# Optimization experiments

Hardware: AMD Instinct MI355X
Metric: run time of the kernel (lower is better)

## Reference

```python
import jax, jax.numpy as jnp
import numpy as np
import math

B, N, M = 128, 32, 64           # batch, num_agents, num_other
OBS, ACT = 128, 16              # obs_input_dim, num_actions
D_QK = 128                      # obs_output_dim (== obs_output_dim_other)
D_AV = 64                       # obs_act_output_dim (== other)
F_IN = OBS + ACT                # obs_act_input_dim = 144


def _xavier(key, shape):
    fan_in, fan_out = shape[0], shape[1]
    limit = math.sqrt(6.0 / (fan_in + fan_out))
    return jax.random.uniform(key, shape, jnp.float32, -limit, limit)


def setup_inputs() -> dict:
    key = jax.random.key(0)
    ks = jax.random.split(key, 13)
    return {
        "states": jax.random.normal(ks[0], (B, N, OBS), jnp.float32),
        "policies": jax.random.uniform(ks[1], (B, N, ACT), jnp.float32),
        "actions": jax.random.uniform(ks[2], (B, N, ACT), jnp.float32),
        "states_other": jax.random.normal(ks[3], (B, M, OBS), jnp.float32),
        "actions_other": jax.random.uniform(ks[4], (B, M, ACT), jnp.float32),
        # weights stored as [in, out] (x @ W == nn.Linear without bias)
        "W_key": _xavier(ks[5], (OBS, D_QK)),
        "W_query": _xavier(ks[6], (OBS, D_QK)),
        "W_av": _xavier(ks[7], (F_IN, D_AV)),
        "W_key_other": _xavier(ks[8], (OBS, D_QK)),
        "W_query_other": _xavier(ks[9], (OBS, D_QK)),
        "W_av_other": _xavier(ks[10], (F_IN, D_AV)),
        "W_f1": _xavier(ks[11], (2 * D_AV, 64)),
        "W_f2": _xavier(ks[12], (64, 1)),
    }


def reference(states, policies, actions, states_other, actions_other,
              W_key, W_query, W_av, W_key_other, W_query_other,
              W_av_other, W_f1, W_f2):
    b, n, _ = states.shape
    obs_actions = jnp.concatenate([states, actions], axis=-1)   # [B,N,F_IN]
    obs_policy = jnp.concatenate([states, policies], axis=-1)   # [B,N,F_IN]

    key_obs = states @ W_key                                    # [B,N,D_QK]
    query_obs = states @ W_query                                # [B,N,D_QK]
    d_k = W_key.shape[1]
    weight = jax.nn.softmax(
        jnp.einsum('bid,bjd->bij', query_obs, key_obs) / math.sqrt(d_k), axis=-1)
    ret_weight = weight

    # place_policies is identity on (j,k): oap[b,j,k] = obs_policy[b,k] if j==k else obs_actions[b,k]
    eye = jnp.eye(n, dtype=states.dtype)[None, :, :, None]       # [1,N,N,1]
    oap = eye * obs_policy[:, None, :, :] + (1.0 - eye) * obs_actions[:, None, :, :]
    attention_values = jnp.tanh(oap @ W_av)                      # [B,N,N,D_AV] (j,k)

    # repeat-mul-sum == weighted reduction over k: wav[b,i,j,d] = sum_k w[b,i,k] av[b,j,k,d]
    wav = jnp.einsum('bik,bjkd->bijd', weight, attention_values)  # [B,N,N,D_AV]

    obs_actions_other = jnp.concatenate([states_other, actions_other], axis=-1)
    keys_other = states_other @ W_key_other                      # [B,M,D_QK]
    query_agent = states @ W_query_other                         # [B,N,D_QK]
    av_other = jnp.tanh(obs_actions_other @ W_av_other)          # [B,M,D_AV]
    d_k_o = W_key_other.shape[1]
    weight_other = jax.nn.softmax(
        jnp.einsum('bid,bmd->bim', query_agent, keys_other) / math.sqrt(d_k_o), axis=-1)
    wav_other = jnp.einsum('bim,bmd->bid', weight_other, av_other)  # [B,N,D_AV]

    # broadcast the per-agent other-branch features across the j axis for the concat
    wav_other_b = jnp.broadcast_to(wav_other[:, :, None, :], wav.shape[:-1] + (wav_other.shape[-1],))
    node_features = jnp.concatenate([wav, wav_other_b], axis=-1)  # [B,N,N,2*D_AV]

    h = jax.nn.leaky_relu(node_features @ W_f1, negative_slope=0.01)
    value = h @ W_f2                                              # [B,N,N,1]
    return value, ret_weight, weight_other
```

## Files before the change

kernel.cpp:

```cpp
#include <hip/hip_runtime.h>
#include <math.h>

#define WS_WQK   0
#define WS_WQKO  16384
#define WS_AVA   32768
#define WS_AVO   294912
#define WS_DPROJ 819200

#define INV_SQRT_DK 0.08838834764831845f

__device__ __forceinline__ float dot4(float4 a, float4 b) {
  return a.x*b.x + a.y*b.y + a.z*b.z + a.w*b.w;
}
__device__ __forceinline__ void fma4(float4& a, const float4 w, const float s) {
  a.x += w.x*s; a.y += w.y*s; a.z += w.z*s; a.w += w.w*s;
}

__global__ __launch_bounds__(256) void k1_pre(
    const float* __restrict__ g_states, const float* __restrict__ g_pol,
    const float* __restrict__ g_act, const float* __restrict__ g_so,
    const float* __restrict__ g_ao,
    const float* __restrict__ Wq, const float* __restrict__ Wk,
    const float* __restrict__ Wqo, const float* __restrict__ Wko,
    const float* __restrict__ W_av, const float* __restrict__ W_avo,
    const float* __restrict__ W_f1, float* __restrict__ ws)
{
  __shared__ __align__(16) float pool[8448];
  const int t = threadIdx.x;
  int blk = blockIdx.x;

  if (blk < 32) {
    const float* A; const float* Bm; float* O;
    if (blk < 16) { A = Wq;  Bm = Wk;  O = ws + WS_WQK; }
    else          { A = Wqo; Bm = Wko; O = ws + WS_WQKO; blk -= 16; }
    const int tr = (blk >> 2) << 5;
    const int tc = (blk & 3) << 5;
    float* sA = pool;
    float* sB = pool + 4224;
    const float4* a4 = (const float4*)(A + tr * 128);
    const float4* b4 = (const float4*)(Bm + tc * 128);
    #pragma unroll
    for (int u = 0; u < 4; ++u) {
      int f = t + u * 256;
      int r = f >> 5, c4 = f & 31;
      *(float4*)(sA + r*132 + c4*4) = a4[f];
      *(float4*)(sB + r*132 + c4*4) = b4[f];
    }
    __syncthreads();
    const int e = t & 31, cl0 = t >> 5;
    float acc[4] = {0,0,0,0};
    #pragma unroll 4
    for (int d4 = 0; d4 < 32; ++d4) {
      float4 bv = *(const float4*)(sB + e*132 + d4*4);
      #pragma unroll
      for (int rr = 0; rr < 4; ++rr) {
        float4 av = *(const float4*)(sA + (cl0 + rr*8)*132 + d4*4);
        acc[rr] += dot4(av, bv);
      }
    }
    #pragma unroll
    for (int rr = 0; rr < 4; ++rr)
      O[(tr + cl0 + rr*8)*128 + tc + e] = acc[rr];
    return;
  }
  blk -= 32;

  if (blk < 128) {
    const int b = blk;
    float* s_pre = pool;
    float* s_dl  = pool + 4224;
    {
      const int wv_  = t >> 6;
      const int ap   = wv_ & 1;
      const int rh   = wv_ >> 1;
      const int lane = t & 63;
      const float* gs = g_states + b*4096 + rh*16*128;
      const float* gt = (ap ? g_pol : g_act) + b*512 + rh*16*16;
      float acc[16];
      #pragma unroll
      for (int r = 0; r < 16; ++r) acc[r] = 0.f;
      #pragma unroll 4
      for (int c4 = 0; c4 < 32; ++c4) {
        const float w0 = W_av[(c4*4+0)*64 + lane];
        const float w1 = W_av[(c4*4+1)*64 + lane];
        const float w2 = W_av[(c4*4+2)*64 + lane];
        const float w3 = W_av[(c4*4+3)*64 + lane];
        #pragma unroll
        for (int r = 0; r < 16; ++r) {
          float4 sv = *(const float4*)(gs + r*128 + c4*4);
          acc[r] += sv.x*w0 + sv.y*w1 + sv.z*w2 + sv.w*w3;
        }
      }
      #pragma unroll
      for (int c4 = 0; c4 < 4; ++c4) {
        const float w0 = W_av[(128 + c4*4+0)*64 + lane];
        const float w1 = W_av[(128 + c4*4+1)*64 + lane];
        const float w2 = W_av[(128 + c4*4+2)*64 + lane];
        const float w3 = W_av[(128 + c4*4+3)*64 + lane];
        #pragma unroll
        for (int r = 0; r < 16; ++r) {
          float4 sv = *(const float4*)(gt + r*16 + c4*4);
          acc[r] += sv.x*w0 + sv.y*w1 + sv.z*w2 + sv.w*w3;
        }
      }
      #pragma unroll
      for (int r = 0; r < 16; ++r)
        s_pre[(rh*16 + r)*132 + ap*64 + lane] = acc[r];
    }
    __syncthreads();
    {
      const int r = t >> 3, d0 = (t & 7) << 3;
      float4 a0 = *(const float4*)(s_pre + r*132 + d0);
      float4 a1 = *(const float4*)(s_pre + r*132 + d0 + 4);
      float4 p0 = *(const float4*)(s_pre + r*132 + 64 + d0);
      float4 p1 = *(const float4*)(s_pre + r*132 + 64 + d0 + 4);
      float4 va0, va1, dl0, dl1;
      va0.x = tanhf(a0.x); va0.y = tanhf(a0.y); va0.z = tanhf(a0.z); va0.w = tanhf(a0.w);
      va1.x = tanhf(a1.x); va1.y = tanhf(a1.y); va1.z = tanhf(a1.z); va1.w = tanhf(a1.w);
      dl0.x = tanhf(p0.x) - va0.x; dl0.y = tanhf(p0.y) - va0.y;
      dl0.z = tanhf(p0.z) - va0.z; dl0.w = tanhf(p0.w) - va0.w;
      dl1.x = tanhf(p1.x) - va1.x; dl1.y = tanhf(p1.y) - va1.y;
      dl1.z = tanhf(p1.z) - va1.z; dl1.w = tanhf(p1.w) - va1.w;
      *(float4*)(ws + WS_AVA + b*2048 + r*64 + d0)     = va0;
      *(float4*)(ws + WS_AVA + b*2048 + r*64 + d0 + 4) = va1;
      *(float4*)(s_dl + r*68 + d0)     = dl0;
      *(float4*)(s_dl + r*68 + d0 + 4) = dl1;
    }
    __syncthreads();
    {
      const int h = t & 63;
      const int j0 = (t >> 6) << 3;
      float acc[8] = {0,0,0,0,0,0,0,0};
      #pragma unroll 4
      for (int d4 = 0; d4 < 16; ++d4) {
        float w0 = W_f1[(d4*4+0)*64 + h];
        float w1 = W_f1[(d4*4+1)*64 + h];
        float w2 = W_f1[(d4*4+2)*64 + h];
        float w3 = W_f1[(d4*4+3)*64 + h];
        #pragma unroll
        for (int q = 0; q < 8; ++q) {
          float4 dv = *(const float4*)(s_dl + (j0+q)*68 + d4*4);
          acc[q] += dv.x*w0 + dv.y*w1 + dv.z*w2 + dv.w*w3;
        }
      }
      #pragma unroll
      for (int q = 0; q < 8; ++q)
        ws[WS_DPROJ + b*2048 + (j0+q)*64 + h] = acc[q];
    }
    return;
  }
  blk -= 128;

  {
    const int b = blk >> 1, m0 = (blk & 1) << 5;
    const int wv_  = t >> 6;
    const int lane = t & 63;
    const float* gso = g_so + (b*64 + m0 + wv_*8) * 128;
    const float* gao = g_ao + (b*64 + m0 + wv_*8) * 16;
    float acc[8];
    #pragma unroll
    for (int r = 0; r < 8; ++r) acc[r] = 0.f;
    #pragma unroll 4
    for (int c4 = 0; c4 < 32; ++c4) {
      const float w0 = W_avo[(c4*4+0)*64 + lane];
      const float w1 = W_avo[(c4*4+1)*64 + lane];
      const float w2 = W_avo[(c4*4+2)*64 + lane];
      const float w3 = W_avo[(c4*4+3)*64 + lane];
      #pragma unroll
      for (int r = 0; r < 8; ++r) {
        float4 sv = *(const float4*)(gso + r*128 + c4*4);
        acc[r] += sv.x*w0 + sv.y*w1 + sv.z*w2 + sv.w*w3;
      }
    }
    #pragma unroll
    for (int c4 = 0; c4 < 4; ++c4) {
      const float w0 = W_avo[(128 + c4*4+0)*64 + lane];
      const float w1 = W_avo[(128 + c4*4+1)*64 + lane];
      const float w2 = W_avo[(128 + c4*4+2)*64 + lane];
      const float w3 = W_avo[(128 + c4*4+3)*64 + lane];
      #pragma unroll
      for (int r = 0; r < 8; ++r) {
        float4 sv = *(const float4*)(gao + r*16 + c4*4);
        acc[r] += sv.x*w0 + sv.y*w1 + sv.z*w2 + sv.w*w3;
      }
    }
    #pragma unroll
    for (int r = 0; r < 8; ++r)
      ws[WS_AVO + b*4096 + (m0 + wv_*8 + r)*64 + lane] = tanhf(acc[r]);
  }
}

__global__ __launch_bounds__(256) void k2_main(
    const float* __restrict__ g_states, const float* __restrict__ g_so,
    const float* __restrict__ W_f1, const float* __restrict__ W_f2,
    const float* __restrict__ ws, float* __restrict__ out)
{
  __shared__ __align__(16) float pool[17472];
  float* s_st   = pool;
  float* s_red  = pool + 4352;
  float* s_avA  = pool + 4352;
  float* s_dp   = pool + 6528;
  float* s_avO  = pool;
  float* s_P    = pool + 12800;
  float* s_w    = pool + 14944;
  float* s_wo   = pool + 15232;
  float* s_S    = pool + 15776;
  float* s_wavo = pool + 16320;
  float* s_base = pool + 16864;
  float* s_wf2  = pool + 17408;

  const int t = threadIdx.x;
  const int b = blockIdx.x >> 2;
  const int i0 = (blockIdx.x & 3) << 3;

  {
    const float4* gs4 = (const float4*)(g_states + b * 4096);
    #pragma unroll
    for (int u = 0; u < 4; ++u) {
      int f = t + u * 256;
      int r = f >> 5, c4 = f & 31;
      *(float4*)(s_st + r*132 + c4*4) = gs4[f];
    }
    if (t < 16) *(float4*)(s_wf2 + t*4) = ((const float4*)W_f2)[t];
  }

  {
    const int wave = t >> 6;
    const int col  = t & 63;
    const float* Wp = (col < 32) ? (ws + WS_WQK + col*4)
                                 : (ws + WS_WQKO + (col-32)*4);
    const float* srow = g_states + b*4096 + i0*128 + wave*32;
    float4 acc[8];
    #pragma unroll
    for (int r = 0; r < 8; ++r) acc[r] = make_float4(0.f,0.f,0.f,0.f);
    #pragma unroll 2
    for (int c4 = 0; c4 < 8; ++c4) {
      float4 sv[8];
      #pragma unroll
      for (int r = 0; r < 8; ++r)
        sv[r] = *(const float4*)(srow + r*128 + c4*4);
      #pragma unroll
      for (int k = 0; k < 4; ++k) {
        float4 wv = *(const float4*)(Wp + (wave*32 + c4*4 + k)*128);
        #pragma unroll
        for (int r = 0; r < 8; ++r)
          fma4(acc[r], wv, ((const float*)&sv[r])[k]);
      }
    }
    #pragma unroll
    for (int r = 0; r < 8; ++r)
      *(float4*)(s_red + ((wave*8 + r)*66 + col)*4) = acc[r];
  }
  __syncthreads();
  {
    const int r = t >> 5, cp = t & 31;
    #pragma unroll
    for (int s2 = 0; s2 < 2; ++s2) {
      const int col = cp*2 + s2;
      float4 a0 = *(const float4*)(s_red + ((0*8 + r)*66 + col)*4);
      float4 a1 = *(const float4*)(s_red + ((1*8 + r)*66 + col)*4);
      float4 a2 = *(const float4*)(s_red + ((2*8 + r)*66 + col)*4);
      float4 a3 = *(const float4*)(s_red + ((3*8 + r)*66 + col)*4);
      float4 s4;
      s4.x = (a0.x + a1.x) + (a2.x + a3.x);
      s4.y = (a0.y + a1.y) + (a2.y + a3.y);
      s4.z = (a0.z + a1.z) + (a2.z + a3.z);
      s4.w = (a0.w + a1.w) + (a2.w + a3.w);
      *(float4*)(s_P + r*268 + col*4) = s4;
    }
  }
  __syncthreads();

  {
    const int r = t >> 5, j = t & 31;
    float acc = 0.f;
    #pragma unroll 8
    for (int e4 = 0; e4 < 32; ++e4) {
      float4 p4  = *(const float4*)(s_P + r*268 + e4*4);
      float4 st4 = *(const float4*)(s_st + j*132 + e4*4);
      acc += dot4(p4, st4);
    }
    acc *= INV_SQRT_DK;
    float mx = acc;
    for (int off = 16; off; off >>= 1) mx = fmaxf(mx, __shfl_xor(mx, off, 32));
    float ev = __expf(acc - mx);
    float sum = ev;
    for (int off = 16; off; off >>= 1) sum += __shfl_xor(sum, off, 32);
    float wn = ev / sum;
    out[131072 + b*1024 + (i0 + r)*32 + j] = wn;
    s_w[r*36 + j] = wn;
  }
  __syncthreads();

  for (int tt = 0; tt < 2; ++tt) {
    const float4* gt4 = (const float4*)(g_so + (b*64 + tt*32) * 128);
    #pragma unroll
    for (int u = 0; u < 4; ++u) {
      int f = t + u * 256;
      int r = f >> 5, c4 = f & 31;
      *(float4*)(s_st + r*132 + c4*4) = gt4[f];
    }
    __syncthreads();
    const int r = t >> 5, m = t & 31;
    float acc = 0.f;
    #pragma unroll 8
    for (int c4 = 0; c4 < 32; ++c4) {
      float4 p4  = *(const float4*)(s_P + r*268 + 128 + c4*4);
      float4 st4 = *(const float4*)(s_st + m*132 + c4*4);
      acc += dot4(p4, st4);
    }
    s_wo[r*68 + tt*32 + m] = acc * INV_SQRT_DK;
    __syncthreads();
  }

  #pragma unroll
  for (int p = 0; p < 2; ++p) {
    const int r = (t >> 6) + (p << 2), l = t & 63;
    float v = s_wo[r*68 + l];
    float mx = v;
    for (int off = 32; off; off >>= 1) mx = fmaxf(mx, __shfl_xor(mx, off, 64));
    float ev = __expf(v - mx);
    float sum = ev;
    for (int off = 32; off; off >>= 1) sum += __shfl_xor(sum, off, 64);
    float wn = ev / sum;
    out[262144 + b*2048 + (i0 + r)*64 + l] = wn;
    s_wo[r*68 + l] = wn;
  }
  #pragma unroll
  for (int u = 0; u < 2; ++u) {
    int f = t + u * 256;
    int k = f >> 4, dq = f & 15;
    *(float4*)(s_avA + k*68 + dq*4) = ((const float4*)(ws + WS_AVA + b*2048))[f];
    *(float4*)(s_dp  + k*68 + dq*4) = ((const float4*)(ws + WS_DPROJ + b*2048))[f];
  }
  #pragma unroll
  for (int u = 0; u < 4; ++u) {
    int f = t + u * 256;
    int m = f >> 4, dq = f & 15;
    *(float4*)(s_avO + m*68 + dq*4) = ((const float4*)(ws + WS_AVO + b*4096))[f];
  }
  __syncthreads();

  if (t < 128) {
    const int i = t >> 4, dq = (t & 15) << 2;
    float4 acc = {0,0,0,0};
    #pragma unroll 4
    for (int k = 0; k < 32; ++k) {
      float4 a4 = *(const float4*)(s_avA + k*68 + dq);
      float wv = s_w[i*36 + k];
      acc.x += wv*a4.x; acc.y += wv*a4.y; acc.z += wv*a4.z; acc.w += wv*a4.w;
    }
    *(float4*)(s_S + i*68 + dq) = acc;
  } else {
    const int tt2 = t - 128;
    const int i = tt2 >> 4, dq = (tt2 & 15) << 2;
    float4 acc = {0,0,0,0};
    #pragma unroll 4
    for (int m = 0; m < 64; ++m) {
      float4 a4 = *(const float4*)(s_avO + m*68 + dq);
      float wv = s_wo[i*68 + m];
      acc.x += wv*a4.x; acc.y += wv*a4.y; acc.z += wv*a4.z; acc.w += wv*a4.w;
    }
    *(float4*)(s_wavo + i*68 + dq) = acc;
  }
  __syncthreads();

  {
    const int h = t & 63, g = (t >> 6) << 1;
    float a0 = 0.f, a1 = 0.f;
    #pragma unroll 4
    for (int d = 0; d < 64; ++d) {
      float w1v = W_f1[d*64 + h];
      float w2v = W_f1[(64 + d)*64 + h];
      a0 += s_S[g*68 + d]*w1v + s_wavo[g*68 + d]*w2v;
      a1 += s_S[(g+1)*68 + d]*w1v + s_wavo[(g+1)*68 + d]*w2v;
    }
    s_base[g*68 + h] = a0;
    s_base[(g+1)*68 + h] = a1;
  }
  __syncthreads();

  {
    const int i = t >> 5, j = t & 31;
    const float wij = s_w[i*36 + j];
    float acc = 0.f;
    #pragma unroll 4
    for (int hq = 0; hq < 16; ++hq) {
      float4 b4 = *(const float4*)(s_base + i*68 + hq*4);
      float4 d4 = *(const float4*)(s_dp + j*68 + hq*4);
      float4 f4 = *(const float4*)(s_wf2 + hq*4);
      float p0 = b4.x + wij*d4.x; p0 = p0 > 0.f ? p0 : 0.01f*p0;
      float p1 = b4.y + wij*d4.y; p1 = p1 > 0.f ? p1 : 0.01f*p1;
      float p2 = b4.z + wij*d4.z; p2 = p2 > 0.f ? p2 : 0.01f*p2;
      float p3 = b4.w + wij*d4.w; p3 = p3 > 0.f ? p3 : 0.01f*p3;
      acc += p0*f4.x + p1*f4.y + p2*f4.z + p3*f4.w;
    }
    out[b*1024 + (i0 + i)*32 + j] = acc;
  }
}

extern "C" void kernel_launch(void* const* d_in, const int* in_sizes, int n_in,
                              void* d_out, int out_size, void* d_ws, size_t ws_size,
                              hipStream_t stream) {
  const float* states        = (const float*)d_in[0];
  const float* policies      = (const float*)d_in[1];
  const float* actions       = (const float*)d_in[2];
  const float* states_other  = (const float*)d_in[3];
  const float* actions_other = (const float*)d_in[4];
  const float* W_key         = (const float*)d_in[5];
  const float* W_query       = (const float*)d_in[6];
  const float* W_av          = (const float*)d_in[7];
  const float* W_key_other   = (const float*)d_in[8];
  const float* W_query_other = (const float*)d_in[9];
  const float* W_av_other    = (const float*)d_in[10];
  const float* W_f1          = (const float*)d_in[11];
  const float* W_f2          = (const float*)d_in[12];
  float* out = (float*)d_out;
  float* ws  = (float*)d_ws;

  k1_pre<<<416, 256, 0, stream>>>(states, policies, actions, states_other,
                                  actions_other, W_query, W_key,
                                  W_query_other, W_key_other, W_av, W_av_other,
                                  W_f1, ws);
  k2_main<<<512, 256, 0, stream>>>(states, states_other, W_f1, W_f2, ws, out);
}
```

Measured before the change: 127.5 us.

## Pre-project attention values through W_f1 in prep kernel, simplify main kernel projection

Uses linearity to move the W_f1 projection of the agent and other-agent attention values into k1, so k2 works directly on projected values and merges two weighted reductions plus a matmul into one pass over shared memory. It also restructures the query/key projection in k2 so that each thread computes one full output column without the cross-wave shared-memory reduction, and it shrinks k2's shared memory. The cost is extra work and larger workspace writes in k1, plus a different floating-point summation order.

New measurement: 132.3 us. +3.8%, slower.

```diff
diff --git a/kernel.cpp b/kernel.cpp
--- a/kernel.cpp
+++ b/kernel.cpp
@@ -1,19 +1,16 @@
 #include <hip/hip_runtime.h>
 #include <math.h>
 
-#define WS_WQK   0
-#define WS_WQKO  16384
-#define WS_AVA   32768
-#define WS_AVO   294912
-#define WS_DPROJ 819200
+#define WS_WQK    0
+#define WS_WQKO   16384
+#define WS_AVAPRJ 32768
+#define WS_DPROJ  294912
+#define WS_AVOPRJ 557056
 
 #define INV_SQRT_DK 0.08838834764831845f
 
 __device__ __forceinline__ float dot4(float4 a, float4 b) {
   return a.x*b.x + a.y*b.y + a.z*b.z + a.w*b.w;
-}
-__device__ __forceinline__ void fma4(float4& a, const float4 w, const float s) {
-  a.x += w.x*s; a.y += w.y*s; a.z += w.z*s; a.w += w.w*s;
 }
 
 __global__ __launch_bounds__(256) void k1_pre(
@@ -25,7 +22,7 @@
     const float* __restrict__ W_av, const float* __restrict__ W_avo,
     const float* __restrict__ W_f1, float* __restrict__ ws)
 {
-  __shared__ __align__(16) float pool[8448];
+  __shared__ __align__(16) float pool[8576];
   const int t = threadIdx.x;
   int blk = blockIdx.x;
 
@@ -68,7 +65,8 @@
   if (blk < 128) {
     const int b = blk;
     float* s_pre = pool;
-    float* s_dl  = pool + 4224;
+    float* s_av  = pool + 4224;
+    float* s_dl  = pool + 6400;
     {
       const int wv_  = t >> 6;
       const int ap   = wv_ & 1;
@@ -121,8 +119,8 @@
       dl0.z = tanhf(p0.z) - va0.z; dl0.w = tanhf(p0.w) - va0.w;
       dl1.x = tanhf(p1.x) - va1.x; dl1.y = tanhf(p1.y) - va1.y;
       dl1.z = tanhf(p1.z) - va1.z; dl1.w = tanhf(p1.w) - va1.w;
-      *(float4*)(ws + WS_AVA + b*2048 + r*64 + d0)     = va0;
-      *(float4*)(ws + WS_AVA + b*2048 + r*64 + d0 + 4) = va1;
+      *(float4*)(s_av + r*68 + d0)     = va0;
+      *(float4*)(s_av + r*68 + d0 + 4) = va1;
       *(float4*)(s_dl + r*68 + d0)     = dl0;
       *(float4*)(s_dl + r*68 + d0 + 4) = dl1;
     }
@@ -130,7 +128,8 @@
     {
       const int h = t & 63;
       const int j0 = (t >> 6) << 3;
-      float acc[8] = {0,0,0,0,0,0,0,0};
+      float da[8] = {0,0,0,0,0,0,0,0};
+      float aa[8] = {0,0,0,0,0,0,0,0};
       #pragma unroll 4
       for (int d4 = 0; d4 < 16; ++d4) {
         float w0 = W_f1[(d4*4+0)*64 + h];
@@ -140,12 +139,16 @@
         #pragma unroll
         for (int q = 0; q < 8; ++q) {
           float4 dv = *(const float4*)(s_dl + (j0+q)*68 + d4*4);
-          acc[q] += dv.x*w0 + dv.y*w1 + dv.z*w2 + dv.w*w3;
+          float4 av = *(const float4*)(s_av + (j0+q)*68 + d4*4);
+          da[q] += dv.x*w0 + dv.y*w1 + dv.z*w2 + dv.w*w3;
+          aa[q] += av.x*w0 + av.y*w1 + av.z*w2 + av.w*w3;
         }
       }
       #pragma unroll
-      for (int q = 0; q < 8; ++q)
-        ws[WS_DPROJ + b*2048 + (j0+q)*64 + h] = acc[q];
+      for (int q = 0; q < 8; ++q) {
+        ws[WS_DPROJ  + b*2048 + (j0+q)*64 + h] = da[q];
+        ws[WS_AVAPRJ + b*2048 + (j0+q)*64 + h] = aa[q];
+      }
     }
     return;
   }
@@ -153,6 +156,7 @@
 
   {
     const int b = blk >> 1, m0 = (blk & 1) << 5;
+    float* s_avo = pool;
     const int wv_  = t >> 6;
     const int lane = t & 63;
     const float* gso = g_so + (b*64 + m0 + wv_*8) * 128;
@@ -186,28 +190,46 @@
     }
     #pragma unroll
     for (int r = 0; r < 8; ++r)
-      ws[WS_AVO + b*4096 + (m0 + wv_*8 + r)*64 + lane] = tanhf(acc[r]);
+      s_avo[(wv_*8 + r)*68 + lane] = tanhf(acc[r]);
+    __syncthreads();
+    {
+      const int h = t & 63;
+      const int j0 = (t >> 6) << 3;
+      float oa[8] = {0,0,0,0,0,0,0,0};
+      #pragma unroll 4
+      for (int d4 = 0; d4 < 16; ++d4) {
+        float w0 = W_f1[(64 + d4*4+0)*64 + h];
+        float w1 = W_f1[(64 + d4*4+1)*64 + h];
+        float w2 = W_f1[(64 + d4*4+2)*64 + h];
+        float w3 = W_f1[(64 + d4*4+3)*64 + h];
+        #pragma unroll
+        for (int q = 0; q < 8; ++q) {
+          float4 ov = *(const float4*)(s_avo + (j0+q)*68 + d4*4);
+          oa[q] += ov.x*w0 + ov.y*w1 + ov.z*w2 + ov.w*w3;
+        }
+      }
+      #pragma unroll
+      for (int q = 0; q < 8; ++q)
+        ws[WS_AVOPRJ + b*4096 + (m0 + j0 + q)*64 + h] = oa[q];
+    }
   }
 }
 
 __global__ __launch_bounds__(256) void k2_main(
     const float* __restrict__ g_states, const float* __restrict__ g_so,
-    const float* __restrict__ W_f1, const float* __restrict__ W_f2,
-    const float* __restrict__ ws, float* __restrict__ out)
+    const float* __restrict__ ws, float* __restrict__ out,
+    const float* __restrict__ W_f2)
 {
-  __shared__ __align__(16) float pool[17472];
+  __shared__ __align__(16) float pool[12288];
   float* s_st   = pool;
-  float* s_red  = pool + 4352;
-  float* s_avA  = pool + 4352;
+  float* s_avOp = pool;
+  float* s_avAp = pool + 4352;
   float* s_dp   = pool + 6528;
-  float* s_avO  = pool;
-  float* s_P    = pool + 12800;
-  float* s_w    = pool + 14944;
-  float* s_wo   = pool + 15232;
-  float* s_S    = pool + 15776;
-  float* s_wavo = pool + 16320;
-  float* s_base = pool + 16864;
-  float* s_wf2  = pool + 17408;
+  float* s_P    = pool + 8704;
+  float* s_w    = pool + 10848;
+  float* s_wo   = pool + 11136;
+  float* s_base = pool + 11680;
+  float* s_wf2  = pool + 12224;
 
   const int t = threadIdx.x;
   const int b = blockIdx.x >> 2;
@@ -221,53 +243,40 @@
       int r = f >> 5, c4 = f & 31;
       *(float4*)(s_st + r*132 + c4*4) = gs4[f];
     }
+    #pragma unroll
+    for (int u = 0; u < 2; ++u) {
+      int f = t + u * 256;
+      int k = f >> 4, dq = f & 15;
+      *(float4*)(s_avAp + k*68 + dq*4) = ((const float4*)(ws + WS_AVAPRJ + b*2048))[f];
+      *(float4*)(s_dp   + k*68 + dq*4) = ((const float4*)(ws + WS_DPROJ  + b*2048))[f];
+    }
     if (t < 16) *(float4*)(s_wf2 + t*4) = ((const float4*)W_f2)[t];
   }
 
   {
-    const int wave = t >> 6;
-    const int col  = t & 63;
-    const float* Wp = (col < 32) ? (ws + WS_WQK + col*4)
-                                 : (ws + WS_WQKO + (col-32)*4);
-    const float* srow = g_states + b*4096 + i0*128 + wave*32;
-    float4 acc[8];
-    #pragma unroll
-    for (int r = 0; r < 8; ++r) acc[r] = make_float4(0.f,0.f,0.f,0.f);
-    #pragma unroll 2
-    for (int c4 = 0; c4 < 8; ++c4) {
+    const int wv_ = t >> 6, lane = t & 63;
+    const int cg  = wv_*64 + lane;
+    const float* Wp = (wv_ < 2) ? (ws + WS_WQK  + cg)
+                                : (ws + WS_WQKO + cg - 128);
+    const float* srow = g_states + b*4096 + i0*128;
+    float acc[8] = {0,0,0,0,0,0,0,0};
+    #pragma unroll 4
+    for (int c4 = 0; c4 < 32; ++c4) {
       float4 sv[8];
       #pragma unroll
       for (int r = 0; r < 8; ++r)
         sv[r] = *(const float4*)(srow + r*128 + c4*4);
       #pragma unroll
-      for (int k = 0; k < 4; ++k) {
-        float4 wv = *(const float4*)(Wp + (wave*32 + c4*4 + k)*128);
+      for (int kk = 0; kk < 4; ++kk) {
+        float wv = Wp[(c4*4 + kk)*128];
         #pragma unroll
         for (int r = 0; r < 8; ++r)
-          fma4(acc[r], wv, ((const float*)&sv[r])[k]);
+          acc[r] += wv * ((const float*)&sv[r])[kk];
       }
     }
     #pragma unroll
     for (int r = 0; r < 8; ++r)
-      *(float4*)(s_red + ((wave*8 + r)*66 + col)*4) = acc[r];
-  }
-  __syncthreads();
-  {
-    const int r = t >> 5, cp = t & 31;
-    #pragma unroll
-    for (int s2 = 0; s2 < 2; ++s2) {
-      const int col = cp*2 + s2;
-      float4 a0 = *(const float4*)(s_red + ((0*8 + r)*66 + col)*4);
-      float4 a1 = *(const float4*)(s_red + ((1*8 + r)*66 + col)*4);
-      float4 a2 = *(const float4*)(s_red + ((2*8 + r)*66 + col)*4);
-      float4 a3 = *(const float4*)(s_red + ((3*8 + r)*66 + col)*4);
-      float4 s4;
-      s4.x = (a0.x + a1.x) + (a2.x + a3.x);
-      s4.y = (a0.y + a1.y) + (a2.y + a3.y);
-      s4.z = (a0.z + a1.z) + (a2.z + a3.z);
-      s4.w = (a0.w + a1.w) + (a2.w + a3.w);
-      *(float4*)(s_P + r*268 + col*4) = s4;
-    }
+      s_P[r*268 + cg] = acc[r];
   }
   __syncthreads();
 
@@ -327,56 +336,41 @@
     s_wo[r*68 + l] = wn;
   }
   #pragma unroll
-  for (int u = 0; u < 2; ++u) {
-    int f = t + u * 256;
-    int k = f >> 4, dq = f & 15;
-    *(float4*)(s_avA + k*68 + dq*4) = ((const float4*)(ws + WS_AVA + b*2048))[f];
-    *(float4*)(s_dp  + k*68 + dq*4) = ((const float4*)(ws + WS_DPROJ + b*2048))[f];
-  }
-  #pragma unroll
   for (int u = 0; u < 4; ++u) {
     int f = t + u * 256;
     int m = f >> 4, dq = f & 15;
-    *(float4*)(s_avO + m*68 + dq*4) = ((const float4*)(ws + WS_AVO + b*4096))[f];
+    *(float4*)(s_avOp + m*68 + dq*4) = ((const float4*)(ws + WS_AVOPRJ + b*4096))[f];
   }
   __syncthreads();
 
-  if (t < 128) {
-    const int i = t >> 4, dq = (t & 15) << 2;
-    float4 acc = {0,0,0,0};
-    #pragma unroll 4
-    for (int k = 0; k < 32; ++k) {
-      float4 a4 = *(const float4*)(s_avA + k*68 + dq);
-      float wv = s_w[i*36 + k];
-      acc.x += wv*a4.x; acc.y += wv*a4.y; acc.z += wv*a4.z; acc.w += wv*a4.w;
-    }
-    *(float4*)(s_S + i*68 + dq) = acc;
-  } else {
-    const int tt2 = t - 128;
-    const int i = tt2 >> 4, dq = (tt2 & 15) << 2;
-    float4 acc = {0,0,0,0};
-    #pragma unroll 4
-    for (int m = 0; m < 64; ++m) {
-      float4 a4 = *(const float4*)(s_avO + m*68 + dq);
-      float wv = s_wo[i*68 + m];
-      acc.x += wv*a4.x; acc.y += wv*a4.y; acc.z += wv*a4.z; acc.w += wv*a4.w;
-    }
-    *(float4*)(s_wavo + i*68 + dq) = acc;
-  }
-  __syncthreads();
-
-  {
-    const int h = t & 63, g = (t >> 6) << 1;
+  {
+    const int g = t >> 6, h = t & 63;
+    const int r0 = g*2, r1 = r0 + 1;
     float a0 = 0.f, a1 = 0.f;
-    #pragma unroll 4
-    for (int d = 0; d < 64; ++d) {
-      float w1v = W_f1[d*64 + h];
-      float w2v = W_f1[(64 + d)*64 + h];
-      a0 += s_S[g*68 + d]*w1v + s_wavo[g*68 + d]*w2v;
-      a1 += s_S[(g+1)*68 + d]*w1v + s_wavo[(g+1)*68 + d]*w2v;
-    }
-    s_base[g*68 + h] = a0;
-    s_base[(g+1)*68 + h] = a1;
+    #pragma unroll 2
+    for (int k4 = 0; k4 < 8; ++k4) {
+      float4 wa = *(const float4*)(s_w + r0*36 + k4*4);
+      float4 wb = *(const float4*)(s_w + r1*36 + k4*4);
+      #pragma unroll
+      for (int kk = 0; kk < 4; ++kk) {
+        float pv = s_avAp[(k4*4 + kk)*68 + h];
+        a0 += ((const float*)&wa)[kk] * pv;
+        a1 += ((const float*)&wb)[kk] * pv;
+      }
+    }
+    #pragma unroll 2
+    for (int m4 = 0; m4 < 16; ++m4) {
+      float4 wa = *(const float4*)(s_wo + r0*68 + m4*4);
+      float4 wb = *(const float4*)(s_wo + r1*68 + m4*4);
+      #pragma unroll
+      for (int kk = 0; kk < 4; ++kk) {
+        float pv = s_avOp[(m4*4 + kk)*68 + h];
+        a0 += ((const float*)&wa)[kk] * pv;
+        a1 += ((const float*)&wb)[kk] * pv;
+      }
+    }
+    s_base[r0*68 + h] = a0;
+    s_base[r1*68 + h] = a1;
   }
   __syncthreads();
 
@@ -422,5 +416,5 @@
                                   actions_other, W_query, W_key,
                                   W_query_other, W_key_other, W_av, W_av_other,
                                   W_f1, ws);
-  k2_main<<<512, 256, 0, stream>>>(states, states_other, W_f1, W_f2, ws, out);
+  k2_main<<<512, 256, 0, stream>>>(states, states_other, ws, out, W_f2);
 }
```

## Drop split-K projection reduction and hoist avA/dproj loads to kernel start

Applied to the files above, without the earlier changes.

The per-block query projection used to split the 128-long K dimension across four waves, writing partial sums to shared memory and reducing them after a barrier. Now each wave owns two rows and computes the full K loop itself, so the reduction buffer and one __syncthreads go away and shared memory shrinks. The avA and dproj workspace loads move to the start of the kernel to overlap with the projection. In exchange each thread does a longer serial loop with less parallelism over K, and it reads more weight data per row computed.

After: 132.3 us. 3.8% more time.

```diff
diff --git a/kernel.cpp b/kernel.cpp
--- a/kernel.cpp
+++ b/kernel.cpp
@@ -153,13 +153,10 @@
 
   {
     const int b = blk >> 1, m0 = (blk & 1) << 5;
-    const int wv_  = t >> 6;
-    const int lane = t & 63;
-    const float* gso = g_so + (b*64 + m0 + wv_*8) * 128;
-    const float* gao = g_ao + (b*64 + m0 + wv_*8) * 16;
-    float acc[8];
-    #pragma unroll
-    for (int r = 0; r < 8; ++r) acc[r] = 0.f;
+    const int rg = t >> 6, lane = t & 63;
+    const float* gso = g_so + (b*64 + m0 + rg*8) * 128;
+    const float* gao = g_ao + (b*64 + m0 + rg*8) * 16;
+    float acc[8] = {0,0,0,0,0,0,0,0};
     #pragma unroll 4
     for (int c4 = 0; c4 < 32; ++c4) {
       const float w0 = W_avo[(c4*4+0)*64 + lane];
@@ -186,7 +183,7 @@
     }
     #pragma unroll
     for (int r = 0; r < 8; ++r)
-      ws[WS_AVO + b*4096 + (m0 + wv_*8 + r)*64 + lane] = tanhf(acc[r]);
+      ws[WS_AVO + b*4096 + (m0 + rg*8 + r)*64 + lane] = tanhf(acc[r]);
   }
 }
 
@@ -195,19 +192,18 @@
     const float* __restrict__ W_f1, const float* __restrict__ W_f2,
     const float* __restrict__ ws, float* __restrict__ out)
 {
-  __shared__ __align__(16) float pool[17472];
+  __shared__ __align__(16) float pool[13376];
   float* s_st   = pool;
-  float* s_red  = pool + 4352;
+  float* s_avO  = pool;
   float* s_avA  = pool + 4352;
   float* s_dp   = pool + 6528;
-  float* s_avO  = pool;
-  float* s_P    = pool + 12800;
-  float* s_w    = pool + 14944;
-  float* s_wo   = pool + 15232;
-  float* s_S    = pool + 15776;
-  float* s_wavo = pool + 16320;
-  float* s_base = pool + 16864;
-  float* s_wf2  = pool + 17408;
+  float* s_P    = pool + 8704;
+  float* s_w    = pool + 10848;
+  float* s_wo   = pool + 11136;
+  float* s_S    = pool + 11680;
+  float* s_wavo = pool + 12224;
+  float* s_base = pool + 12768;
+  float* s_wf2  = pool + 13312;
 
   const int t = threadIdx.x;
   const int b = blockIdx.x >> 2;
@@ -221,53 +217,37 @@
       int r = f >> 5, c4 = f & 31;
       *(float4*)(s_st + r*132 + c4*4) = gs4[f];
     }
+    #pragma unroll
+    for (int u = 0; u < 2; ++u) {
+      int f = t + u * 256;
+      int k = f >> 4, dq = f & 15;
+      *(float4*)(s_avA + k*68 + dq*4) = ((const float4*)(ws + WS_AVA + b*2048))[f];
+      *(float4*)(s_dp  + k*68 + dq*4) = ((const float4*)(ws + WS_DPROJ + b*2048))[f];
+    }
     if (t < 16) *(float4*)(s_wf2 + t*4) = ((const float4*)W_f2)[t];
   }
 
   {
-    const int wave = t >> 6;
-    const int col  = t & 63;
-    const float* Wp = (col < 32) ? (ws + WS_WQK + col*4)
-                                 : (ws + WS_WQKO + (col-32)*4);
-    const float* srow = g_states + b*4096 + i0*128 + wave*32;
-    float4 acc[8];
-    #pragma unroll
-    for (int r = 0; r < 8; ++r) acc[r] = make_float4(0.f,0.f,0.f,0.f);
-    #pragma unroll 2
-    for (int c4 = 0; c4 < 8; ++c4) {
-      float4 sv[8];
-      #pragma unroll
-      for (int r = 0; r < 8; ++r)
-        sv[r] = *(const float4*)(srow + r*128 + c4*4);
-      #pragma unroll
-      for (int k = 0; k < 4; ++k) {
-        float4 wv = *(const float4*)(Wp + (wave*32 + c4*4 + k)*128);
-        #pragma unroll
-        for (int r = 0; r < 8; ++r)
-          fma4(acc[r], wv, ((const float*)&sv[r])[k]);
-      }
-    }
-    #pragma unroll
-    for (int r = 0; r < 8; ++r)
-      *(float4*)(s_red + ((wave*8 + r)*66 + col)*4) = acc[r];
-  }
-  __syncthreads();
-  {
-    const int r = t >> 5, cp = t & 31;
-    #pragma unroll
-    for (int s2 = 0; s2 < 2; ++s2) {
-      const int col = cp*2 + s2;
-      float4 a0 = *(const float4*)(s_red + ((0*8 + r)*66 + col)*4);
-      float4 a1 = *(const float4*)(s_red + ((1*8 + r)*66 + col)*4);
-      float4 a2 = *(const float4*)(s_red + ((2*8 + r)*66 + col)*4);
-      float4 a3 = *(const float4*)(s_red + ((3*8 + r)*66 + col)*4);
-      float4 s4;
-      s4.x = (a0.x + a1.x) + (a2.x + a3.x);
-      s4.y = (a0.y + a1.y) + (a2.y + a3.y);
-      s4.z = (a0.z + a1.z) + (a2.z + a3.z);
-      s4.w = (a0.w + a1.w) + (a2.w + a3.w);
-      *(float4*)(s_P + r*268 + col*4) = s4;
-    }
+    const int wv = t >> 6, lane = t & 63;
+    const int r0 = wv * 2;
+    const float* Wbase = (lane < 32) ? (ws + WS_WQK  + lane*4)
+                                     : (ws + WS_WQKO + (lane-32)*4);
+    const float* srow0 = g_states + b*4096 + (i0 + r0)*128;
+    const float* srow1 = srow0 + 128;
+    float4 a0 = {0,0,0,0}, a1 = {0,0,0,0};
+    #pragma unroll 4
+    for (int c4 = 0; c4 < 32; ++c4) {
+      float4 s0 = *(const float4*)(srow0 + c4*4);
+      float4 s1 = *(const float4*)(srow1 + c4*4);
+      #pragma unroll
+      for (int kk = 0; kk < 4; ++kk) {
+        float4 wv4 = *(const float4*)(Wbase + (c4*4 + kk)*128);
+        fma4(a0, wv4, ((const float*)&s0)[kk]);
+        fma4(a1, wv4, ((const float*)&s1)[kk]);
+      }
+    }
+    *(float4*)(s_P + r0*268 + lane*4)       = a0;
+    *(float4*)(s_P + (r0+1)*268 + lane*4)   = a1;
   }
   __syncthreads();
 
@@ -325,13 +305,6 @@
     float wn = ev / sum;
     out[262144 + b*2048 + (i0 + r)*64 + l] = wn;
     s_wo[r*68 + l] = wn;
-  }
-  #pragma unroll
-  for (int u = 0; u < 2; ++u) {
-    int f = t + u * 256;
-    int k = f >> 4, dq = f & 15;
-    *(float4*)(s_avA + k*68 + dq*4) = ((const float4*)(ws + WS_AVA + b*2048))[f];
-    *(float4*)(s_dp  + k*68 + dq*4) = ((const float4*)(ws + WS_DPROJ + b*2048))[f];
   }
   #pragma unroll
   for (int u = 0; u < 4; ++u) {
```
